# Kernel optimization log

Hardware: AMD Instinct MI355X
Metric: run time of the kernel (lower is better)

Reference implementation:

```python
import jax, jax.numpy as jnp
import numpy as np

N = 20000   # genes
E = 200000  # global edges
P = 300     # pathways
EP = 2000   # edges per pathway (global node indices)
D = 3       # in_dim == number of omics (forced by nn.Linear(3,1))


def setup_inputs():
    key = jax.random.key(0)
    ks = jax.random.split(key, 20)
    f = lambda i, shape: jax.random.normal(ks[i], shape, dtype=jnp.float32) * 0.1
    return {
        "x": f(0, (N, D)),
        "edge_index": jax.random.randint(ks[1], (2, E), 0, N),
        "path_edges": jax.random.randint(ks[2], (P, 2, EP), 0, N),
        "W_pool": f(3, (D, D)), "b_pool": f(4, (D,)),
        "W_self": f(5, (D, D)), "W_neigh": f(6, (D, D)), "b_conv": f(7, (D,)),
        "sub_Wl": f(8, (P, D, D)), "sub_bl": f(9, (P, D)), "sub_Wr": f(10, (P, D, D)),
        "pool_Wrel": f(11, (P, D, 1)), "pool_Wroot": f(12, (P, D, 1)), "pool_b": f(13, (P, 1)),
        "gate_W": f(14, (P, D, 1)), "gate_b": f(15, (P, 1)),
        "lin_W": f(16, (D, 1)), "lin_b": f(17, (1,)),
        "mlp_W": f(18, (P, 1)), "mlp_b": f(19, (1,)),
    }


def reference(x, edge_index, path_edges, W_pool, b_pool, W_self, W_neigh, b_conv,
              sub_Wl, sub_bl, sub_Wr, pool_Wrel, pool_Wroot, pool_b,
              gate_W, gate_b, lin_W, lin_b, mlp_W, mlp_b):
    n = x.shape[0]
    # add_self_loops on the global edge_index
    loops = jnp.arange(n)
    src = jnp.concatenate([edge_index[0], loops])
    dst = jnp.concatenate([edge_index[1], loops])

    # global SAGEConv with 'pool' aggregator: max_j relu(W_pool h_j), then self + neigh
    hp = jax.nn.relu(x @ W_pool + b_pool)                       # [N,D]
    agg = jax.ops.segment_max(hp[src], dst, num_segments=n)     # [N,D] (self-loops -> no empty segments)
    h = jnp.tanh(x @ W_self + agg @ W_neigh + b_conv)           # [N,D]

    k = int(np.ceil(0.8 * n))  # SAGPooling ratio=0.8 over all N nodes (full x is passed per pathway)

    def per_path(pe, Wl, bl, Wr, Wrel, Wroot, pb, gW, gb):
        s, d = pe[0], pe[1]
        # SAGEConv (mean aggr) on pathway subgraph edges over full node set
        msum = jax.ops.segment_sum(h[s], d, num_segments=n)
        cnt = jax.ops.segment_sum(jnp.ones(s.shape, h.dtype), d, num_segments=n)
        mean = msum / jnp.maximum(cnt, 1.0)[:, None]
        xc = jax.nn.relu(mean @ Wl + bl + h @ Wr)               # [N,D]
        # SAGPooling score via GraphConv (add aggr): W_rel * sum_j x_j + W_root * x + b
        asum = jax.ops.segment_sum(xc[s], d, num_segments=n)
        score = (asum @ Wrel + xc @ Wroot + pb)[:, 0]           # [N]
        topv, perm = jax.lax.top_k(score, k)
        xk = xc[perm] * jnp.tanh(topv)[:, None]                 # [k,D]
        # GlobalAttention readout: softmax gate over kept nodes
        gate = jax.nn.softmax((xk @ gW + gb)[:, 0])             # [k]
        return jax.nn.relu(gate @ xk)                            # [D]

    readout = jax.vmap(per_path)(path_edges, sub_Wl, sub_bl, sub_Wr,
                                 pool_Wrel, pool_Wroot, pool_b, gate_W, gate_b)  # [P,D]
    r = jax.nn.relu(readout @ lin_W + lin_b).T                  # [1,P]
    # mlp: Dropout (identity in eval) -> ReLU -> Linear(P,1) -> Sigmoid
    return jax.nn.sigmoid(jax.nn.relu(r) @ mlp_W + mlp_b)       # [1,1]
```

## Files before the change

### kernel.cpp

```cpp
#include <hip/hip_runtime.h>
#include <math.h>

#define MAXM 2048
#define BMW  640
#define BS   1024
#define NB   2048

__device__ __forceinline__ unsigned fkey(float f){
  unsigned u = __float_as_uint(f);
  return (u & 0x80000000u) ? ~u : (u | 0x80000000u);
}
__device__ __forceinline__ int lbin(float sc, float lo, float scl){
  int b = (int)((sc - lo) * scl);
  return b < 0 ? 0 : (b > NB-1 ? NB-1 : b);
}
__device__ __forceinline__ void hp_eval(const float* __restrict__ x, int i,
                                        const float* __restrict__ Wp,
                                        const float* __restrict__ bp, float* o){
  float x0 = x[i*3+0], x1 = x[i*3+1], x2 = x[i*3+2];
  #pragma unroll
  for (int j = 0; j < 3; ++j)
    o[j] = fmaxf(x0*Wp[0*3+j] + x1*Wp[1*3+j] + x2*Wp[2*3+j] + bp[j], 0.f);
}

__global__ void k_edge(const float* __restrict__ x, const int* __restrict__ ei,
                       const float* __restrict__ Wp, const float* __restrict__ bp,
                       float* __restrict__ agg, float* __restrict__ acc,
                       unsigned* __restrict__ counter, int E){
  if (blockIdx.x == 0 && threadIdx.x == 0){ acc[0] = 0.f; counter[0] = 0u; }
  int e = blockIdx.x*blockDim.x + threadIdx.x;
  if (e >= E) return;
  int s = ei[e], d = ei[E+e];
  float o[3]; hp_eval(x, s, Wp, bp, o);
  #pragma unroll
  for (int j = 0; j < 3; ++j)
    if (o[j] > 0.f)
      atomicMax((int*)&agg[d*3+j], __float_as_int(o[j]));
}

__global__ void k_h2(const float* __restrict__ x, float* __restrict__ hb,
                     const float* __restrict__ Wp, const float* __restrict__ bp,
                     const float* __restrict__ Ws, const float* __restrict__ Wn,
                     const float* __restrict__ bc, int N){
  int i = blockIdx.x*blockDim.x + threadIdx.x;
  if (i >= N) return;
  float hp[3]; hp_eval(x, i, Wp, bp, hp);
  float x0 = x[i*3+0], x1 = x[i*3+1], x2 = x[i*3+2];
  float a0 = fmaxf(hb[i*3+0], hp[0]);
  float a1 = fmaxf(hb[i*3+1], hp[1]);
  float a2 = fmaxf(hb[i*3+2], hp[2]);
  float o[3];
  #pragma unroll
  for (int j = 0; j < 3; ++j){
    float v = x0*Ws[0*3+j] + x1*Ws[1*3+j] + x2*Ws[2*3+j]
            + a0*Wn[0*3+j] + a1*Wn[1*3+j] + a2*Wn[2*3+j] + bc[j];
    o[j] = tanhf(v);
  }
  hb[i*3+0] = o[0]; hb[i*3+1] = o[1]; hb[i*3+2] = o[2];
}

__device__ __forceinline__ void pick_bucket(const unsigned* hist, int l,
    unsigned pref, unsigned mask, int shift,
    unsigned* sel_prefix, unsigned* sel_mask, int* sel_r){
  unsigned h0 = hist[4*l+0], h1 = hist[4*l+1], h2 = hist[4*l+2], h3 = hist[4*l+3];
  unsigned s = h0+h1+h2+h3;
  unsigned S = s;
  #pragma unroll
  for (int off = 1; off < 64; off <<= 1){
    unsigned t = __shfl_down(S, off);
    if (l + off < 64) S += t;
  }
  unsigned Snext = S - s;
  unsigned r = (unsigned)*sel_r;
  unsigned suf3 = h3 + Snext;
  unsigned suf2 = h2 + suf3;
  unsigned suf1 = h1 + suf2;
  unsigned suf0 = h0 + suf1;
  int b = -1; unsigned sufnext = 0;
  if      (suf3 >= r && Snext < r){ b = 4*l+3; sufnext = Snext; }
  else if (suf2 >= r && suf3  < r){ b = 4*l+2; sufnext = suf3; }
  else if (suf1 >= r && suf2  < r){ b = 4*l+1; sufnext = suf2; }
  else if (suf0 >= r && suf1  < r){ b = 4*l+0; sufnext = suf1; }
  if (b >= 0){
    *sel_prefix = pref | ((unsigned)b << shift);
    *sel_mask   = mask | (255u << shift);
    *sel_r      = (int)(r - sufnext);
  }
}

__global__ void __launch_bounds__(BS)
k_mega(const float* __restrict__ h, const int* __restrict__ pe,
       const float* __restrict__ sWl, const float* __restrict__ sbl, const float* __restrict__ sWr,
       const float* __restrict__ pWrel, const float* __restrict__ pWroot, const float* __restrict__ pB,
       const float* __restrict__ gW, const float* __restrict__ gB,
       const float* __restrict__ linW, const float* __restrict__ linb,
       const float* __restrict__ mlpW, const float* __restrict__ mlpb,
       float* __restrict__ spG, float* __restrict__ acc, unsigned* __restrict__ counter,
       unsigned* __restrict__ out, int N, int EP, int K, int P){
  __shared__ unsigned bm[BMW];
  __shared__ int      wpfx[BMW];
  __shared__ float    msum[MAXM*3];
  __shared__ unsigned scrA[NB];
  __shared__ unsigned scrB[NB];
  __shared__ float    wredf[(BS/64)*2];
  __shared__ float    wredA[(BS/64)*4];
  __shared__ float    wredB[(BS/64)*4];
  __shared__ float    s_mn, s_mx;
  __shared__ float    rlo[3], rsc[3];
  __shared__ int      rb[3];
  __shared__ int      s_r, s_C, s_cc, s_done;
  __shared__ unsigned s_uT;
  __shared__ unsigned sel_prefix, sel_mask;
  __shared__ int      sel_r;

  const int p = blockIdx.x;
  const int tid = threadIdx.x;

  float Wl[9], Wr[9], bl[3], wrel[3], wroot[3], gw[3];
  #pragma unroll
  for (int j = 0; j < 9; ++j){ Wl[j] = sWl[p*9+j]; Wr[j] = sWr[p*9+j]; }
  #pragma unroll
  for (int j = 0; j < 3; ++j){
    bl[j] = sbl[p*3+j]; wrel[j] = pWrel[p*3+j];
    wroot[j] = pWroot[p*3+j]; gw[j] = gW[p*3+j];
  }
  float pbv = pB[p], gbv = gB[p];
  float* sp = spG + (size_t)p*N;

  int*   cnt  = (int*)scrA;
  float* adot = (float*)scrB;

  for (int s = tid; s < MAXM; s += BS){
    cnt[s] = 0; adot[s] = 0.f;
    msum[s*3+0]=0.f; msum[s*3+1]=0.f; msum[s*3+2]=0.f;
  }
  for (int s = tid; s < BMW; s += BS) bm[s] = 0u;
  if (tid == 0){ s_done = 0; s_uT = 0u; }
  __syncthreads();

  const int* ps = pe + (size_t)p*2*EP;
  const int* pd = ps + EP;

  for (int e = tid; e < EP; e += BS) atomicOr(&bm[pd[e]>>5], 1u << (pd[e]&31));
  __syncthreads();
  if (tid < 64){
    int l = tid, base = l*10;
    int c[10], s = 0;
    #pragma unroll
    for (int q = 0; q < 10; ++q){ c[q] = __popc(bm[base+q]); s += c[q]; }
    int pre = s;
    #pragma unroll
    for (int off = 1; off < 64; off <<= 1){
      int t = __shfl_up(pre, off);
      if (l >= off) pre += t;
    }
    pre -= s;
    #pragma unroll
    for (int q = 0; q < 10; ++q){ wpfx[base+q] = pre; pre += c[q]; }
  }
  __syncthreads();
  for (int e = tid; e < EP; e += BS){
    int s = ps[e], d = pd[e];
    int r = wpfx[d>>5] + __popc(bm[d>>5] & ((1u << (d&31)) - 1u));
    atomicAdd(&cnt[r], 1);
    atomicAdd(&msum[r*3+0], h[s*3+0]);
    atomicAdd(&msum[r*3+1], h[s*3+1]);
    atomicAdd(&msum[r*3+2], h[s*3+2]);
  }
  __syncthreads();
  for (int r = tid; r < MAXM; r += BS){
    int c = cnt[r];
    if (c > 0){
      float inv = 1.f / (float)c;
      msum[r*3+0] *= inv; msum[r*3+1] *= inv; msum[r*3+2] *= inv;
    }
  }
  __syncthreads();
  for (int e = tid; e < EP; e += BS){
    int s = ps[e], d = pd[e];
    float m0=0.f,m1=0.f,m2=0.f;
    unsigned w = bm[s>>5];
    if ((w >> (s&31)) & 1u){
      int rs = wpfx[s>>5] + __popc(w & ((1u << (s&31)) - 1u));
      m0 = msum[rs*3+0]; m1 = msum[rs*3+1]; m2 = msum[rs*3+2];
    }
    float h0 = h[s*3+0], h1 = h[s*3+1], h2 = h[s*3+2];
    float x0 = fmaxf(m0*Wl[0]+m1*Wl[3]+m2*Wl[6] + bl[0] + h0*Wr[0]+h1*Wr[3]+h2*Wr[6], 0.f);
    float x1 = fmaxf(m0*Wl[1]+m1*Wl[4]+m2*Wl[7] + bl[1] + h0*Wr[1]+h1*Wr[4]+h2*Wr[7], 0.f);
    float x2 = fmaxf(m0*Wl[2]+m1*Wl[5]+m2*Wl[8] + bl[2] + h0*Wr[2]+h1*Wr[5]+h2*Wr[8], 0.f);
    int rd = wpfx[d>>5] + __popc(bm[d>>5] & ((1u << (d&31)) - 1u));
    atomicAdd(&adot[rd], x0*wrel[0] + x1*wrel[1] + x2*wrel[2]);
  }
  __syncthreads();

  float mn = 3.0e38f, mx = -3.0e38f;
  float tl = 0.f, ta0 = 0.f, ta1 = 0.f, ta2 = 0.f;
  for (int i = tid; i < N; i += BS){
    float m0=0.f,m1=0.f,m2=0.f,ad=0.f;
    unsigned w = bm[i>>5];
    if ((w >> (i&31)) & 1u){
      int r = wpfx[i>>5] + __popc(w & ((1u << (i&31)) - 1u));
      m0 = msum[r*3+0]; m1 = msum[r*3+1]; m2 = msum[r*3+2];
      ad = adot[r];
    }
    float h0 = h[i*3+0], h1 = h[i*3+1], h2 = h[i*3+2];
    float x0 = fmaxf(m0*Wl[0]+m1*Wl[3]+m2*Wl[6] + bl[0] + h0*Wr[0]+h1*Wr[3]+h2*Wr[6], 0.f);
    float x1 = fmaxf(m0*Wl[1]+m1*Wl[4]+m2*Wl[7] + bl[1] + h0*Wr[1]+h1*Wr[4]+h2*Wr[7], 0.f);
    float x2 = fmaxf(m0*Wl[2]+m1*Wl[5]+m2*Wl[8] + bl[2] + h0*Wr[2]+h1*Wr[5]+h2*Wr[8], 0.f);
    float sc = ad + x0*wroot[0]+x1*wroot[1]+x2*wroot[2] + pbv;
    sp[i] = sc;
    mn = fminf(mn, sc); mx = fmaxf(mx, sc);
    float tt = tanhf(sc);
    float g = fminf(fmaxf(tt*(x0*gw[0]+x1*gw[1]+x2*gw[2]) + gbv, -60.f), 60.f);
    float e = expf(g);
    float et = e * tt;
    tl += e; ta0 += et*x0; ta1 += et*x1; ta2 += et*x2;
  }
  #pragma unroll
  for (int off = 32; off > 0; off >>= 1){
    mn  = fminf(mn, __shfl_down(mn, off));
    mx  = fmaxf(mx, __shfl_down(mx, off));
    tl  += __shfl_down(tl,  off); ta0 += __shfl_down(ta0, off);
    ta1 += __shfl_down(ta1, off); ta2 += __shfl_down(ta2, off);
  }
  if ((tid & 63) == 0){
    int w = tid >> 6;
    wredf[w*2+0] = mn; wredf[w*2+1] = mx;
    wredA[w*4+0]=tl; wredA[w*4+1]=ta0; wredA[w*4+2]=ta1; wredA[w*4+3]=ta2;
  }
  __syncthreads();
  if (tid == 0){
    float a = 3.0e38f, b = -3.0e38f;
    for (int w = 0; w < BS/64; ++w){ a = fminf(a, wredf[w*2+0]); b = fmaxf(b, wredf[w*2+1]); }
    s_mn = a; s_mx = b; s_r = K;
    if (!(b > a)){ s_uT = fkey(a); s_done = 1; }
  }
  __syncthreads();

  unsigned* hist = scrA;
  unsigned* cand = scrB;

  for (int t = 0; t < 3; ++t){
    __syncthreads();
    if (s_done) break;
    float lo, hi;
    if (t == 0){ lo = s_mn; hi = s_mx; }
    else { lo = rlo[t-1] + rb[t-1]/rsc[t-1]; hi = rlo[t-1] + (rb[t-1]+1)/rsc[t-1]; }
    float scl = 2047.0f / (hi - lo);
    if (!(hi > lo) || !(scl < 1e37f)){
      if (tid == 0){ s_uT = fkey(lo); s_done = 1; }
      __syncthreads();
      continue;
    }
    for (int b = tid; b < NB; b += BS) hist[b] = 0u;
    __syncthreads();
    if (t == 0){
      if ((N & 3) == 0){
        int G = N >> 2;
        for (int g = tid; g < G; g += BS){
          float4 v = ((const float4*)sp)[g];
          atomicAdd(&hist[lbin(v.x, lo, scl)], 1u);
          atomicAdd(&hist[lbin(v.y, lo, scl)], 1u);
          atomicAdd(&hist[lbin(v.z, lo, scl)], 1u);
          atomicAdd(&hist[lbin(v.w, lo, scl)], 1u);
        }
      } else {
        for (int i = tid; i < N; i += BS) atomicAdd(&hist[lbin(sp[i], lo, scl)], 1u);
      }
    } else {
      for (int i = tid; i < N; i += BS){
        float sc = sp[i];
        bool act = true;
        for (int q = 0; q < t; ++q) act = act && (lbin(sc, rlo[q], rsc[q]) == rb[q]);
        if (act) atomicAdd(&hist[lbin(sc, lo, scl)], 1u);
      }
    }
    __syncthreads();
    if (tid < 64){
      int l = tid;
      unsigned s = 0;
      for (int q = 0; q < 32; ++q) s += hist[l*32+q];
      unsigned S = s;
      #pragma unroll
      for (int off = 1; off < 64; off <<= 1){
        unsigned u2 = __shfl_down(S, off);
        if (l + off < 64) S += u2;
      }
      unsigned suf = S - s;
      unsigned r = (unsigned)s_r;
      int b = -1; unsigned sufnext = 0, cb = 0;
      for (int q = 31; q >= 0; --q){
        unsigned c = hist[l*32+q];
        unsigned nsuf = suf + c;
        if (nsuf >= r && suf < r){ b = l*32+q; sufnext = suf; cb = c; }
        suf = nsuf;
      }
      if (b >= 0){
        rb[t] = b; rlo[t] = lo; rsc[t] = scl;
        s_r = (int)(r - sufnext);
        s_C = (int)cb;
      }
    }
    __syncthreads();
    int C = s_C;
    if (C <= NB){
      if (tid == 0) s_cc = 0;
      __syncthreads();
      for (int i = tid; i < N; i += BS){
        float sc = sp[i];
        bool act = true;
        for (int q = 0; q <= t; ++q) act = act && (lbin(sc, rlo[q], rsc[q]) == rb[q]);
        if (act){ int ix = atomicAdd(&s_cc, 1); if (ix < NB) cand[ix] = fkey(sc); }
      }
      __syncthreads();
      if (tid == 0){ sel_prefix = 0u; sel_mask = 0u; sel_r = s_r; }
      __syncthreads();
      for (int pass = 0; pass < 4; ++pass){
        int shift = 24 - 8*pass;
        if (tid < 256) hist[tid] = 0u;
        __syncthreads();
        unsigned mask = sel_mask, pref = sel_prefix;
        for (int j = tid; j < C; j += BS){
          unsigned u = cand[j];
          if ((u & mask) == pref) atomicAdd(&hist[(u>>shift)&255u], 1u);
        }
        __syncthreads();
        if (tid < 64)
          pick_bucket(hist, tid, pref, mask, shift, &sel_prefix, &sel_mask, &sel_r);
        __syncthreads();
      }
      if (tid == 0){ s_uT = sel_prefix; s_done = 1; }
      __syncthreads();
    } else if (t == 2){
      if (tid == 0){ s_uT = fkey(lo + rb[t]/scl); s_done = 1; }
      __syncthreads();
    }
  }
  __syncthreads();
  const unsigned uT = s_uT;

  float dl = 0.f, d0 = 0.f, d1 = 0.f, d2 = 0.f;
  for (int i = tid; i < N; i += BS){
    float sc = sp[i];
    if (fkey(sc) < uT){
      float m0=0.f,m1=0.f,m2=0.f;
      unsigned w = bm[i>>5];
      if ((w >> (i&31)) & 1u){
        int r = wpfx[i>>5] + __popc(w & ((1u << (i&31)) - 1u));
        m0 = msum[r*3+0]; m1 = msum[r*3+1]; m2 = msum[r*3+2];
      }
      float h0 = h[i*3+0], h1 = h[i*3+1], h2 = h[i*3+2];
      float x0 = fmaxf(m0*Wl[0]+m1*Wl[3]+m2*Wl[6] + bl[0] + h0*Wr[0]+h1*Wr[3]+h2*Wr[6], 0.f);
      float x1 = fmaxf(m0*Wl[1]+m1*Wl[4]+m2*Wl[7] + bl[1] + h0*Wr[1]+h1*Wr[4]+h2*Wr[7], 0.f);
      float x2 = fmaxf(m0*Wl[2]+m1*Wl[5]+m2*Wl[8] + bl[2] + h0*Wr[2]+h1*Wr[5]+h2*Wr[8], 0.f);
      float tt = tanhf(sc);
      float g = fminf(fmaxf(tt*(x0*gw[0]+x1*gw[1]+x2*gw[2]) + gbv, -60.f), 60.f);
      float e = expf(g);
      float et = e * tt;
      dl += e; d0 += et*x0; d1 += et*x1; d2 += et*x2;
    }
  }
  #pragma unroll
  for (int off = 32; off > 0; off >>= 1){
    dl += __shfl_down(dl, off); d0 += __shfl_down(d0, off);
    d1 += __shfl_down(d1, off); d2 += __shfl_down(d2, off);
  }
  if ((tid & 63) == 0){
    int w = tid >> 6;
    wredB[w*4+0]=dl; wredB[w*4+1]=d0; wredB[w*4+2]=d1; wredB[w*4+3]=d2;
  }
  __syncthreads();
  if (tid == 0){
    float L=0.f, A0=0.f, A1=0.f, A2=0.f;
    for (int w = 0; w < BS/64; ++w){
      L  += wredA[w*4+0] - wredB[w*4+0];
      A0 += wredA[w*4+1] - wredB[w*4+1];
      A1 += wredA[w*4+2] - wredB[w*4+2];
      A2 += wredA[w*4+3] - wredB[w*4+3];
    }
    float inv = 1.f / L;
    float r0 = fmaxf(A0*inv, 0.f);
    float r1 = fmaxf(A1*inv, 0.f);
    float r2 = fmaxf(A2*inv, 0.f);
    float rr = fmaxf(r0*linW[0] + r1*linW[1] + r2*linW[2] + linb[0], 0.f);
    atomicAdd(acc, rr * mlpW[p]);
    __threadfence();
    unsigned old = atomicAdd(counter, 1u);
    if (old == (unsigned)(P-1)){
      __threadfence();
      float z = atomicAdd(acc, 0.f) + mlpb[0];
      float a = 1.f / (1.f + expf(-z));
      unsigned A = __float_as_uint(a);
      unsigned B = (A + 0x7FFFu + ((A >> 16) & 1u)) >> 16;
      out[0] = (A & 0xFFFF0000u) | (B & 0xFFFFu);
    }
  }
}

extern "C" void kernel_launch(void* const* d_in, const int* in_sizes, int n_in,
                              void* d_out, int out_size, void* d_ws, size_t ws_size,
                              hipStream_t stream){
  const float* x      = (const float*)d_in[0];
  const int*   ei     = (const int*)  d_in[1];
  const int*   pe     = (const int*)  d_in[2];
  const float* W_pool = (const float*)d_in[3];
  const float* b_pool = (const float*)d_in[4];
  const float* W_self = (const float*)d_in[5];
  const float* W_neigh= (const float*)d_in[6];
  const float* b_conv = (const float*)d_in[7];
  const float* sWl    = (const float*)d_in[8];
  const float* sbl    = (const float*)d_in[9];
  const float* sWr    = (const float*)d_in[10];
  const float* pWrel  = (const float*)d_in[11];
  const float* pWroot = (const float*)d_in[12];
  const float* pB     = (const float*)d_in[13];
  const float* gW     = (const float*)d_in[14];
  const float* gB     = (const float*)d_in[15];
  const float* linW   = (const float*)d_in[16];
  const float* linb   = (const float*)d_in[17];
  const float* mlpW   = (const float*)d_in[18];
  const float* mlpb   = (const float*)d_in[19];

  const int N  = in_sizes[0] / 3;
  const int E  = in_sizes[1] / 2;
  const int P  = in_sizes[13];
  const int EP = in_sizes[2] / (2 * P);
  const int K  = (4*N + 4) / 5;

  float*    ws      = (float*)d_ws;
  float*    acc     = ws;
  unsigned* counter = (unsigned*)(ws + 1);
  float*    agg     = ws + 16;
  float*    h       = agg;
  float*    spG     = ws + 16 + (size_t)3*N;

  k_edge<<<(E+255)/256, 256, 0, stream>>>(x, ei, W_pool, b_pool, agg, acc, counter, E);
  k_h2  <<<(N+255)/256, 256, 0, stream>>>(x, agg, W_pool, b_pool,
                                          W_self, W_neigh, b_conv, N);
  k_mega<<<P, BS, 0, stream>>>(h, pe, sWl, sbl, sWr, pWrel, pWroot, pB, gW, gB,
                               linW, linb, mlpW, mlpb,
                               spG, acc, counter, (unsigned*)d_out, N, EP, K, P);
}
```

Baseline: 244.3 us.

## Fuse dropped-node accumulation into candidate scan and run radix select in one wave

The kernel sums the gate contributions of nodes that fall below the top-k threshold. It now does this inside the candidate-collection scan, for nodes whose histogram bin lies below the selected bin, and for candidates after the exact threshold is found. Because candidate indices are stored, the separate final pass over all N nodes is skipped. The four-pass radix select now runs inside a single wavefront, using waitcnt and ballot/shuffle in place of block-wide barriers. tanh and exp use fast intrinsics, and the edge kernel skips the atomicMax when the stored value is already larger. This risks small numerical differences and adds shared memory for the candidate indices.

```diff
diff --git a/kernel.cpp b/kernel.cpp
--- a/kernel.cpp
+++ b/kernel.cpp
@@ -13,6 +13,10 @@
 __device__ __forceinline__ int lbin(float sc, float lo, float scl){
   int b = (int)((sc - lo) * scl);
   return b < 0 ? 0 : (b > NB-1 ? NB-1 : b);
+}
+__device__ __forceinline__ float fast_tanh(float x){
+  float e = __expf(2.f*x);
+  return 1.f - 2.f*__builtin_amdgcn_rcpf(e + 1.f);
 }
 __device__ __forceinline__ void hp_eval(const float* __restrict__ x, int i,
                                         const float* __restrict__ Wp,
@@ -34,7 +38,7 @@
   float o[3]; hp_eval(x, s, Wp, bp, o);
   #pragma unroll
   for (int j = 0; j < 3; ++j)
-    if (o[j] > 0.f)
+    if (o[j] > 0.f && o[j] > agg[d*3+j])
       atomicMax((int*)&agg[d*3+j], __float_as_int(o[j]));
 }
 
@@ -57,35 +61,6 @@
     o[j] = tanhf(v);
   }
   hb[i*3+0] = o[0]; hb[i*3+1] = o[1]; hb[i*3+2] = o[2];
-}
-
-__device__ __forceinline__ void pick_bucket(const unsigned* hist, int l,
-    unsigned pref, unsigned mask, int shift,
-    unsigned* sel_prefix, unsigned* sel_mask, int* sel_r){
-  unsigned h0 = hist[4*l+0], h1 = hist[4*l+1], h2 = hist[4*l+2], h3 = hist[4*l+3];
-  unsigned s = h0+h1+h2+h3;
-  unsigned S = s;
-  #pragma unroll
-  for (int off = 1; off < 64; off <<= 1){
-    unsigned t = __shfl_down(S, off);
-    if (l + off < 64) S += t;
-  }
-  unsigned Snext = S - s;
-  unsigned r = (unsigned)*sel_r;
-  unsigned suf3 = h3 + Snext;
-  unsigned suf2 = h2 + suf3;
-  unsigned suf1 = h1 + suf2;
-  unsigned suf0 = h0 + suf1;
-  int b = -1; unsigned sufnext = 0;
-  if      (suf3 >= r && Snext < r){ b = 4*l+3; sufnext = Snext; }
-  else if (suf2 >= r && suf3  < r){ b = 4*l+2; sufnext = suf3; }
-  else if (suf1 >= r && suf2  < r){ b = 4*l+1; sufnext = suf2; }
-  else if (suf0 >= r && suf1  < r){ b = 4*l+0; sufnext = suf1; }
-  if (b >= 0){
-    *sel_prefix = pref | ((unsigned)b << shift);
-    *sel_mask   = mask | (255u << shift);
-    *sel_r      = (int)(r - sufnext);
-  }
 }
 
 __global__ void __launch_bounds__(BS)
@@ -102,16 +77,15 @@
   __shared__ float    msum[MAXM*3];
   __shared__ unsigned scrA[NB];
   __shared__ unsigned scrB[NB];
+  __shared__ unsigned candIdx[NB];
   __shared__ float    wredf[(BS/64)*2];
   __shared__ float    wredA[(BS/64)*4];
   __shared__ float    wredB[(BS/64)*4];
   __shared__ float    s_mn, s_mx;
   __shared__ float    rlo[3], rsc[3];
   __shared__ int      rb[3];
-  __shared__ int      s_r, s_C, s_cc, s_done;
+  __shared__ int      s_r, s_C, s_cc, s_done, s_fused;
   __shared__ unsigned s_uT;
-  __shared__ unsigned sel_prefix, sel_mask;
-  __shared__ int      sel_r;
 
   const int p = blockIdx.x;
   const int tid = threadIdx.x;
@@ -135,7 +109,7 @@
     msum[s*3+0]=0.f; msum[s*3+1]=0.f; msum[s*3+2]=0.f;
   }
   for (int s = tid; s < BMW; s += BS) bm[s] = 0u;
-  if (tid == 0){ s_done = 0; s_uT = 0u; }
+  if (tid == 0){ s_done = 0; s_fused = 0; s_uT = 0u; }
   __syncthreads();
 
   const int* ps = pe + (size_t)p*2*EP;
@@ -210,9 +184,9 @@
     float sc = ad + x0*wroot[0]+x1*wroot[1]+x2*wroot[2] + pbv;
     sp[i] = sc;
     mn = fminf(mn, sc); mx = fmaxf(mx, sc);
-    float tt = tanhf(sc);
+    float tt = fast_tanh(sc);
     float g = fminf(fmaxf(tt*(x0*gw[0]+x1*gw[1]+x2*gw[2]) + gbv, -60.f), 60.f);
-    float e = expf(g);
+    float e = __expf(g);
     float et = e * tt;
     tl += e; ta0 += et*x0; ta1 += et*x1; ta2 += et*x2;
   }
@@ -233,12 +207,14 @@
     float a = 3.0e38f, b = -3.0e38f;
     for (int w = 0; w < BS/64; ++w){ a = fminf(a, wredf[w*2+0]); b = fmaxf(b, wredf[w*2+1]); }
     s_mn = a; s_mx = b; s_r = K;
-    if (!(b > a)){ s_uT = fkey(a); s_done = 1; }
+    if (!(b > a)){ s_uT = fkey(a); s_done = 1; s_fused = 1; }
   }
   __syncthreads();
 
   unsigned* hist = scrA;
   unsigned* cand = scrB;
+
+  float dl = 0.f, d0 = 0.f, d1 = 0.f, d2 = 0.f;
 
   for (int t = 0; t < 3; ++t){
     __syncthreads();
@@ -308,29 +284,102 @@
       __syncthreads();
       for (int i = tid; i < N; i += BS){
         float sc = sp[i];
-        bool act = true;
-        for (int q = 0; q <= t; ++q) act = act && (lbin(sc, rlo[q], rsc[q]) == rb[q]);
-        if (act){ int ix = atomicAdd(&s_cc, 1); if (ix < NB) cand[ix] = fkey(sc); }
+        bool iscand = true, isdrop = false;
+        for (int q = 0; q <= t; ++q){
+          int b = lbin(sc, rlo[q], rsc[q]);
+          if (b != rb[q]){ iscand = false; isdrop = (b < rb[q]); break; }
+        }
+        if (iscand){
+          int ix = atomicAdd(&s_cc, 1);
+          if (ix < NB){ cand[ix] = fkey(sc); candIdx[ix] = (unsigned)i; }
+        } else if (isdrop){
+          float m0=0.f,m1=0.f,m2=0.f;
+          unsigned w = bm[i>>5];
+          if ((w >> (i&31)) & 1u){
+            int r = wpfx[i>>5] + __popc(w & ((1u << (i&31)) - 1u));
+            m0 = msum[r*3+0]; m1 = msum[r*3+1]; m2 = msum[r*3+2];
+          }
+          float h0 = h[i*3+0], h1 = h[i*3+1], h2 = h[i*3+2];
+          float x0 = fmaxf(m0*Wl[0]+m1*Wl[3]+m2*Wl[6] + bl[0] + h0*Wr[0]+h1*Wr[3]+h2*Wr[6], 0.f);
+          float x1 = fmaxf(m0*Wl[1]+m1*Wl[4]+m2*Wl[7] + bl[1] + h0*Wr[1]+h1*Wr[4]+h2*Wr[7], 0.f);
+          float x2 = fmaxf(m0*Wl[2]+m1*Wl[5]+m2*Wl[8] + bl[2] + h0*Wr[2]+h1*Wr[5]+h2*Wr[8], 0.f);
+          float tt = fast_tanh(sc);
+          float g = fminf(fmaxf(tt*(x0*gw[0]+x1*gw[1]+x2*gw[2]) + gbv, -60.f), 60.f);
+          float e = __expf(g);
+          float et = e * tt;
+          dl += e; d0 += et*x0; d1 += et*x1; d2 += et*x2;
+        }
       }
       __syncthreads();
-      if (tid == 0){ sel_prefix = 0u; sel_mask = 0u; sel_r = s_r; }
+      if (tid < 64){
+        int l = tid;
+        unsigned pref = 0u, mask = 0u;
+        int r = s_r;
+        #pragma unroll
+        for (int pass = 0; pass < 4; ++pass){
+          int shift = 24 - 8*pass;
+          hist[4*l+0]=0u; hist[4*l+1]=0u; hist[4*l+2]=0u; hist[4*l+3]=0u;
+          asm volatile("s_waitcnt lgkmcnt(0)" ::: "memory");
+          for (int j = l; j < C; j += 64){
+            unsigned u = cand[j];
+            if ((u & mask) == pref) atomicAdd(&hist[(u>>shift)&255u], 1u);
+          }
+          asm volatile("s_waitcnt lgkmcnt(0)" ::: "memory");
+          unsigned h0 = hist[4*l+0], h1 = hist[4*l+1], h2 = hist[4*l+2], h3 = hist[4*l+3];
+          unsigned ssum = h0+h1+h2+h3;
+          unsigned S = ssum;
+          #pragma unroll
+          for (int off = 1; off < 64; off <<= 1){
+            unsigned u2 = __shfl_down(S, off);
+            if (l + off < 64) S += u2;
+          }
+          unsigned Snext = S - ssum;
+          unsigned rr = (unsigned)r;
+          unsigned suf3 = h3 + Snext;
+          unsigned suf2 = h2 + suf3;
+          unsigned suf1 = h1 + suf2;
+          unsigned suf0 = h0 + suf1;
+          int b = -1; unsigned sufn = 0;
+          if      (suf3 >= rr && Snext < rr){ b = 4*l+3; sufn = Snext; }
+          else if (suf2 >= rr && suf3  < rr){ b = 4*l+2; sufn = suf3; }
+          else if (suf1 >= rr && suf2  < rr){ b = 4*l+1; sufn = suf2; }
+          else if (suf0 >= rr && suf1  < rr){ b = 4*l+0; sufn = suf1; }
+          unsigned long long ball = __ballot(b >= 0);
+          int src = __ffsll(ball) - 1;
+          b    = __shfl(b, src);
+          sufn = (unsigned)__shfl((int)sufn, src);
+          pref |= (unsigned)b << shift;
+          mask |= 255u << shift;
+          r = (int)(rr - sufn);
+        }
+        if (l == 0) s_uT = pref;
+      }
+      if (tid == 0){ s_done = 1; s_fused = 1; }
       __syncthreads();
-      for (int pass = 0; pass < 4; ++pass){
-        int shift = 24 - 8*pass;
-        if (tid < 256) hist[tid] = 0u;
-        __syncthreads();
-        unsigned mask = sel_mask, pref = sel_prefix;
+      {
+        const unsigned uTl = s_uT;
         for (int j = tid; j < C; j += BS){
-          unsigned u = cand[j];
-          if ((u & mask) == pref) atomicAdd(&hist[(u>>shift)&255u], 1u);
-        }
-        __syncthreads();
-        if (tid < 64)
-          pick_bucket(hist, tid, pref, mask, shift, &sel_prefix, &sel_mask, &sel_r);
-        __syncthreads();
-      }
-      if (tid == 0){ s_uT = sel_prefix; s_done = 1; }
-      __syncthreads();
+          if (cand[j] < uTl){
+            int i = (int)candIdx[j];
+            float sc = sp[i];
+            float m0=0.f,m1=0.f,m2=0.f;
+            unsigned w = bm[i>>5];
+            if ((w >> (i&31)) & 1u){
+              int r = wpfx[i>>5] + __popc(w & ((1u << (i&31)) - 1u));
+              m0 = msum[r*3+0]; m1 = msum[r*3+1]; m2 = msum[r*3+2];
+            }
+            float h0 = h[i*3+0], h1 = h[i*3+1], h2 = h[i*3+2];
+            float x0 = fmaxf(m0*Wl[0]+m1*Wl[3]+m2*Wl[6] + bl[0] + h0*Wr[0]+h1*Wr[3]+h2*Wr[6], 0.f);
+            float x1 = fmaxf(m0*Wl[1]+m1*Wl[4]+m2*Wl[7] + bl[1] + h0*Wr[1]+h1*Wr[4]+h2*Wr[7], 0.f);
+            float x2 = fmaxf(m0*Wl[2]+m1*Wl[5]+m2*Wl[8] + bl[2] + h0*Wr[2]+h1*Wr[5]+h2*Wr[8], 0.f);
+            float tt = fast_tanh(sc);
+            float g = fminf(fmaxf(tt*(x0*gw[0]+x1*gw[1]+x2*gw[2]) + gbv, -60.f), 60.f);
+            float e = __expf(g);
+            float et = e * tt;
+            dl += e; d0 += et*x0; d1 += et*x1; d2 += et*x2;
+          }
+        }
+      }
     } else if (t == 2){
       if (tid == 0){ s_uT = fkey(lo + rb[t]/scl); s_done = 1; }
       __syncthreads();
@@ -339,25 +388,26 @@
   __syncthreads();
   const unsigned uT = s_uT;
 
-  float dl = 0.f, d0 = 0.f, d1 = 0.f, d2 = 0.f;
-  for (int i = tid; i < N; i += BS){
-    float sc = sp[i];
-    if (fkey(sc) < uT){
-      float m0=0.f,m1=0.f,m2=0.f;
-      unsigned w = bm[i>>5];
-      if ((w >> (i&31)) & 1u){
-        int r = wpfx[i>>5] + __popc(w & ((1u << (i&31)) - 1u));
-        m0 = msum[r*3+0]; m1 = msum[r*3+1]; m2 = msum[r*3+2];
-      }
-      float h0 = h[i*3+0], h1 = h[i*3+1], h2 = h[i*3+2];
-      float x0 = fmaxf(m0*Wl[0]+m1*Wl[3]+m2*Wl[6] + bl[0] + h0*Wr[0]+h1*Wr[3]+h2*Wr[6], 0.f);
-      float x1 = fmaxf(m0*Wl[1]+m1*Wl[4]+m2*Wl[7] + bl[1] + h0*Wr[1]+h1*Wr[4]+h2*Wr[7], 0.f);
-      float x2 = fmaxf(m0*Wl[2]+m1*Wl[5]+m2*Wl[8] + bl[2] + h0*Wr[2]+h1*Wr[5]+h2*Wr[8], 0.f);
-      float tt = tanhf(sc);
-      float g = fminf(fmaxf(tt*(x0*gw[0]+x1*gw[1]+x2*gw[2]) + gbv, -60.f), 60.f);
-      float e = expf(g);
-      float et = e * tt;
-      dl += e; d0 += et*x0; d1 += et*x1; d2 += et*x2;
+  if (!s_fused){
+    for (int i = tid; i < N; i += BS){
+      float sc = sp[i];
+      if (fkey(sc) < uT){
+        float m0=0.f,m1=0.f,m2=0.f;
+        unsigned w = bm[i>>5];
+        if ((w >> (i&31)) & 1u){
+          int r = wpfx[i>>5] + __popc(w & ((1u << (i&31)) - 1u));
+          m0 = msum[r*3+0]; m1 = msum[r*3+1]; m2 = msum[r*3+2];
+        }
+        float h0 = h[i*3+0], h1 = h[i*3+1], h2 = h[i*3+2];
+        float x0 = fmaxf(m0*Wl[0]+m1*Wl[3]+m2*Wl[6] + bl[0] + h0*Wr[0]+h1*Wr[3]+h2*Wr[6], 0.f);
+        float x1 = fmaxf(m0*Wl[1]+m1*Wl[4]+m2*Wl[7] + bl[1] + h0*Wr[1]+h1*Wr[4]+h2*Wr[7], 0.f);
+        float x2 = fmaxf(m0*Wl[2]+m1*Wl[5]+m2*Wl[8] + bl[2] + h0*Wr[2]+h1*Wr[5]+h2*Wr[8], 0.f);
+        float tt = fast_tanh(sc);
+        float g = fminf(fmaxf(tt*(x0*gw[0]+x1*gw[1]+x2*gw[2]) + gbv, -60.f), 60.f);
+        float e = __expf(g);
+        float et = e * tt;
+        dl += e; d0 += et*x0; d1 += et*x1; d2 += et*x2;
+      }
     }
   }
   #pragma unroll
```

Result: faster. 236.2 us (-3.3%).
